# Performance work log

Hardware: AMD Instinct MI355X
Metric: run time of the kernel (lower is better)

The kernel has to match this reference:

```python
import jax, jax.numpy as jnp
import numpy as np

N_ENTITIES = 100000
EMBED = 64
BATCH = 4096
TEMPERATURE = 0.2


def _infonce(v1, v2, temperature):
    # v1, v2: [B, d]
    B = v1.shape[0]
    sim11 = v1 @ v1.T  # [B,B]
    sim22 = v2 @ v2.T
    sim12 = v1 @ v2.T
    eye = jnp.eye(B, dtype=bool)
    neg_inf = jnp.float32(-jnp.inf)
    sim11 = jnp.where(eye, neg_inf, sim11)
    sim22 = jnp.where(eye, neg_inf, sim22)
    logits1 = jnp.concatenate([sim12, sim11], axis=-1)          # [B,2B]
    logits2 = jnp.concatenate([sim22, sim12.T], axis=-1)        # [B,2B]
    logits = jnp.concatenate([logits1, logits2], axis=0) / temperature  # [2B,2B]
    targets = jnp.arange(2 * B)
    logp = jax.nn.log_softmax(logits, axis=-1)
    return -jnp.mean(jnp.take_along_axis(logp, targets[:, None], axis=-1))


def setup_inputs() -> dict:
    key = jax.random.key(0)
    k1, k2, k3, k4, k5, k6 = jax.random.split(key, 6)
    return {
        "input_u_list": jax.random.randint(k1, (BATCH,), 0, N_ENTITIES),
        "input_i_list": jax.random.randint(k2, (BATCH,), 0, N_ENTITIES),
        "u_sub1_embeddings": jax.random.normal(k3, (N_ENTITIES, EMBED), dtype=jnp.float32),
        "i_sub1_embeddings": jax.random.normal(k4, (N_ENTITIES, EMBED), dtype=jnp.float32),
        "u_sub2_embeddings": jax.random.normal(k5, (N_ENTITIES, EMBED), dtype=jnp.float32),
        "i_sub2_embeddings": jax.random.normal(k6, (N_ENTITIES, EMBED), dtype=jnp.float32),
    }


def reference(input_u_list, input_i_list, u_sub1_embeddings, i_sub1_embeddings,
              u_sub2_embeddings, i_sub2_embeddings):
    # user branch: gather + L2-normalize
    u1 = u_sub1_embeddings[input_u_list]
    u2 = u_sub2_embeddings[input_u_list]
    u1 = u1 / jnp.linalg.norm(u1, axis=1, keepdims=True)
    u2 = u2 / jnp.linalg.norm(u2, axis=1, keepdims=True)
    user_cl_loss = _infonce(u1, u2, TEMPERATURE)
    # item branch: gather only (the original does NOT normalize items)
    i1 = i_sub1_embeddings[input_i_list]
    i2 = i_sub2_embeddings[input_i_list]
    item_cl_loss = _infonce(i1, i2, TEMPERATURE)
    return user_cl_loss + item_cl_loss
```

## Files before the change

### kernel.cpp

```cpp
#include <hip/hip_runtime.h>
#include <hip/hip_bf16.h>
#include <math.h>

#define B_SZ   4096
#define D      64
#define RPB    8192
#define NCHUNK 8
#define TPC    8
#define NPART  16
#define LN2    0.69314718055994531f
#define PRESCALE 2.6857914f

typedef __attribute__((ext_vector_type(8))) short  bf16x8;
typedef __attribute__((ext_vector_type(4))) float  f32x4;

__device__ __forceinline__ float fexp2(float x) { return __builtin_amdgcn_exp2f(x); }


__global__ __launch_bounds__(256) void gather_kernel(
    const int* __restrict__ u_idx, const int* __restrict__ i_idx,
    const float* __restrict__ u1e, const float* __restrict__ i1e,
    const float* __restrict__ u2e, const float* __restrict__ i2e,
    __hip_bfloat16* __restrict__ Xbf, float* __restrict__ dots)
{
    const int tid  = threadIdx.x;
    const int wave = tid >> 6, lane = tid & 63;
    const int g      = blockIdx.x * 4 + wave;
    const int branch = g >> 12;
    const int i      = g & (B_SZ - 1);
    const int idx    = (branch == 0) ? u_idx[i] : i_idx[i];
    const float* s1  = (branch == 0) ? u1e : i1e;
    const float* s2  = (branch == 0) ? u2e : i2e;

    float v1 = s1[(size_t)idx * D + lane];
    float v2 = s2[(size_t)idx * D + lane];
    if (branch == 0) {
        float a = v1 * v1, b = v2 * v2;
        #pragma unroll
        for (int o = 32; o > 0; o >>= 1) {
            a += __shfl_xor(a, o, 64);
            b += __shfl_xor(b, o, 64);
        }
        v1 *= rsqrtf(a);
        v2 *= rsqrtf(b);
    }
    float p = v1 * v2;
    #pragma unroll
    for (int o = 32; o > 0; o >>= 1) p += __shfl_xor(p, o, 64);
    if (lane == 0) dots[g] = p;

    const size_t row1 = (size_t)branch * RPB + i;
    Xbf[row1 * D + lane]          = __float2bfloat16(v1 * PRESCALE);
    Xbf[(row1 + B_SZ) * D + lane] = __float2bfloat16(v2 * PRESCALE);
}

template<int IS_USER>
__device__ __forceinline__ void gram_body(
    const __hip_bfloat16* __restrict__ Xb, float2* __restrict__ P)
{
    const int tid   = threadIdx.x;
    const int bx    = blockIdx.x;
    const int chunk = blockIdx.y;
    const int r0    = bx * 128;

    const int wave = tid >> 6, lane = tid & 63;
    const int wm = wave >> 1, wn = wave & 1;
    const int quad = lane >> 4, tx = lane & 15;

    bf16x8 afr[4][2];
    const __hip_bfloat16* Ap = Xb + (size_t)(r0 + wm * 64 + tx) * D + quad * 8;
    #pragma unroll
    for (int mt = 0; mt < 4; ++mt)
        #pragma unroll
        for (int ks = 0; ks < 2; ++ks)
            afr[mt][ks] = *(const bf16x8*)(Ap + mt * 16 * D + ks * 32);

    float m_run[16], s_run[16];
    #pragma unroll
    for (int r = 0; r < 16; ++r) { m_run[r] = -INFINITY; s_run[r] = 0.f; }

    const int lrq  = wm * 64 + quad * 4;
    const int lcol = wn * 64 + tx;

    const __hip_bfloat16* Bbase =
        Xb + (size_t)(chunk * TPC * 128 + wn * 64 + tx) * D + quad * 8;

    for (int t = 0; t < TPC; ++t) {
        const int ct = chunk * TPC + t;
        const __hip_bfloat16* Bp = Bbase + (size_t)t * 128 * D;

        bf16x8 b0[4], b1[4];
        #pragma unroll
        for (int nt = 0; nt < 4; ++nt) {
            b0[nt] = *(const bf16x8*)(Bp + nt * 16 * D);
            b1[nt] = *(const bf16x8*)(Bp + nt * 16 * D + 32);
        }

        f32x4 acc[4][4];
        const f32x4 z = {0.f, 0.f, 0.f, 0.f};
        #pragma unroll
        for (int nt = 0; nt < 4; ++nt)
            #pragma unroll
            for (int mt = 0; mt < 4; ++mt)
                acc[mt][nt] = __builtin_amdgcn_mfma_f32_16x16x32_bf16(afr[mt][0], b0[nt], z, 0, 0, 0);
        #pragma unroll
        for (int nt = 0; nt < 4; ++nt)
            #pragma unroll
            for (int mt = 0; mt < 4; ++mt)
                acc[mt][nt] = __builtin_amdgcn_mfma_f32_16x16x32_bf16(afr[mt][1], b1[nt], acc[mt][nt], 0, 0, 0);

        const bool diag = (ct == bx);
        #pragma unroll
        for (int mt = 0; mt < 4; ++mt) {
            #pragma unroll
            for (int rr = 0; rr < 4; ++rr) {
                float y0 = acc[mt][0][rr], y1 = acc[mt][1][rr],
                      y2 = acc[mt][2][rr], y3 = acc[mt][3][rr];
                if (diag) {
                    const int dr = lrq + mt * 16 + rr - lcol;
                    if (dr == 0)  y0 = -INFINITY;
                    if (dr == 16) y1 = -INFINITY;
                    if (dr == 32) y2 = -INFINITY;
                    if (dr == 48) y3 = -INFINITY;
                }
                const int r = mt * 4 + rr;
                if (IS_USER) {
                    s_run[r] += fexp2(y0) + fexp2(y1) + fexp2(y2) + fexp2(y3);
                } else {
                    float mx   = fmaxf(fmaxf(y0, y1), fmaxf(y2, y3));
                    float newm = fmaxf(m_run[r], mx);
                    s_run[r] = s_run[r] * fexp2(m_run[r] - newm)
                             + fexp2(y0 - newm) + fexp2(y1 - newm)
                             + fexp2(y2 - newm) + fexp2(y3 - newm);
                    m_run[r] = newm;
                }
            }
        }
    }

    #pragma unroll
    for (int r = 0; r < 16; ++r) {
        float m = IS_USER ? 0.f : m_run[r];
        float s = s_run[r];
        #pragma unroll
        for (int o = 1; o < 16; o <<= 1) {
            if (IS_USER) {
                s += __shfl_xor(s, o, 64);
            } else {
                float om = __shfl_xor(m, o, 64);
                float os = __shfl_xor(s, o, 64);
                float M  = fmaxf(m, om);
                s = s * fexp2(m - M) + os * fexp2(om - M);
                m = M;
            }
        }
        if (tx == 0) {
            const int grow = r0 + wm * 64 + (r >> 2) * 16 + quad * 4 + (r & 3);
            P[(size_t)grow * NPART + chunk * 2 + wn] = make_float2(m, s);
        }
    }
}

__global__ __launch_bounds__(256, 3) void gram_lse_fused(
    const __hip_bfloat16* __restrict__ Xb0, float2* __restrict__ P0)
{
    const int branch = blockIdx.z;
    const __hip_bfloat16* Xb = Xb0 + (size_t)branch * RPB * D;
    float2* P = P0 + (size_t)branch * RPB * NPART;
    if (branch == 0) gram_body<1>(Xb, P);
    else             gram_body<0>(Xb, P);
}

__global__ __launch_bounds__(256) void merge_kernel(
    const float2* __restrict__ P, const float* __restrict__ dots,
    float* __restrict__ out)
{
    __shared__ float red[4];
    const int tid  = threadIdx.x;
    const int wave = tid >> 6, lane = tid & 63;

    float vsum = 0.f;
    #pragma unroll
    for (int k = 0; k < 8; ++k) {
        const int vb  = blockIdx.x * 8 + k;
        const int gw  = vb * 4 + wave;
        const int row = gw * 4 + (lane >> 4);
        const int c   = lane & 15;

        float2 p = P[(size_t)row * NPART + c];
        float m = p.x, s = p.y;
        #pragma unroll
        for (int o = 1; o < 16; o <<= 1) {
            float om = __shfl_xor(m, o, 64);
            float os = __shfl_xor(s, o, 64);
            float M  = fmaxf(m, om);
            s = s * fexp2(m - M) + os * fexp2(om - M);
            m = M;
        }

        if ((lane & 15) == 0)
            vsum += LN2 * (m + log2f(s)) * (1.0f / (float)RPB);
        if (tid < 8)
            vsum -= dots[vb * 8 + tid] * (5.0f / (float)B_SZ);
    }

    float v = vsum;
    #pragma unroll
    for (int o = 32; o > 0; o >>= 1) v += __shfl_xor(v, o, 64);
    if (lane == 0) red[wave] = v;
    __syncthreads();
    if (tid == 0)
        atomicAdd(out, red[0] + red[1] + red[2] + red[3]);
}

extern "C" void kernel_launch(void* const* d_in, const int* in_sizes, int n_in,
                              void* d_out, int out_size, void* d_ws, size_t ws_size,
                              hipStream_t stream) {
    const int*   u_idx = (const int*)d_in[0];
    const int*   i_idx = (const int*)d_in[1];
    const float* u1e   = (const float*)d_in[2];
    const float* i1e   = (const float*)d_in[3];
    const float* u2e   = (const float*)d_in[4];
    const float* i2e   = (const float*)d_in[5];
    float* out = (float*)d_out;

    __hip_bfloat16* Xbf = (__hip_bfloat16*)d_ws;
    float*  dots = (float*)((char*)d_ws + 2 * RPB * D * 2);
    float2* P    = (float2*)((char*)dots + RPB * sizeof(float));

    hipMemsetAsync(out, 0, sizeof(float), stream);

    gather_kernel<<<dim3(2048), dim3(256), 0, stream>>>(
        u_idx, i_idx, u1e, i1e, u2e, i2e, Xbf, dots);
    gram_lse_fused<<<dim3(64, NCHUNK, 2), dim3(256), 0, stream>>>(Xbf, P);
    merge_kernel<<<dim3(128), dim3(256), 0, stream>>>(P, dots, out);
}
```

Before: 173.3 us.

## Stage B tiles through double-buffered swizzled LDS with async global-to-LDS loads

In the gram kernel, each B column tile is now loaded once per block into LDS with global_load_lds, instead of every wave reading it straight from global memory. Two 16KB buffers let the next tile's load overlap the MFMA and exp work on the current one, and the row layout is XOR-swizzled to avoid bank conflicts. The grid is also rearranged so the user and item branches interleave along blockIdx.x. In exchange the kernel uses 32KB of shared memory per block, adds a barrier per tile, and forces the tile loop not to unroll, which may lower occupancy.

After: 169.2 us. 2.4% less time.

```diff
diff --git a/kernel.cpp b/kernel.cpp
--- a/kernel.cpp
+++ b/kernel.cpp
@@ -16,6 +16,12 @@
 
 __device__ __forceinline__ float fexp2(float x) { return __builtin_amdgcn_exp2f(x); }
 
+typedef const __attribute__((address_space(1))) unsigned int* gptr_t;
+typedef __attribute__((address_space(3))) unsigned int* lptr_t;
+__device__ __forceinline__ void stage16(const void* g, void* l) {
+    __builtin_amdgcn_global_load_lds((gptr_t)g, (lptr_t)l, 16, 0, 0);
+}
+
 
 __global__ __launch_bounds__(256) void gather_kernel(
     const int* __restrict__ u_idx, const int* __restrict__ i_idx,
@@ -56,10 +62,10 @@
 
 template<int IS_USER>
 __device__ __forceinline__ void gram_body(
-    const __hip_bfloat16* __restrict__ Xb, float2* __restrict__ P)
+    const __hip_bfloat16* __restrict__ Xb, float2* __restrict__ P,
+    const int bx, char* sm)
 {
     const int tid   = threadIdx.x;
-    const int bx    = blockIdx.x;
     const int chunk = blockIdx.y;
     const int r0    = bx * 128;
 
@@ -67,6 +73,18 @@
     const int wm = wave >> 1, wn = wave & 1;
     const int quad = lane >> 4, tx = lane & 15;
 
+    const int srow_b = wave * 32 + (lane >> 3);
+    const int scb    = ((lane & 7) * 16) ^ ((lane >> 3) << 4);
+    const char* Xbytes = (const char*)Xb;
+
+    {
+        const char* src = Xbytes + (size_t)(chunk * TPC) * 16384;
+        #pragma unroll
+        for (int k = 0; k < 4; ++k)
+            stage16(src + (srow_b + k * 8) * 128 + scb,
+                    sm + wave * 4096 + k * 1024);
+    }
+
     bf16x8 afr[4][2];
     const __hip_bfloat16* Ap = Xb + (size_t)(r0 + wm * 64 + tx) * D + quad * 8;
     #pragma unroll
@@ -82,18 +100,31 @@
     const int lrq  = wm * 64 + quad * 4;
     const int lcol = wn * 64 + tx;
 
-    const __hip_bfloat16* Bbase =
-        Xb + (size_t)(chunk * TPC * 128 + wn * 64 + tx) * D + quad * 8;
-
+    const int rbase = (wn * 64 + tx) * 128;
+    const int key   = (tx & 7) << 4;
+    const int cb0   = (quad * 16) ^ key;
+    const int cb1   = (64 + quad * 16) ^ key;
+
+    __syncthreads();
+
+    #pragma unroll 1
     for (int t = 0; t < TPC; ++t) {
-        const int ct = chunk * TPC + t;
-        const __hip_bfloat16* Bp = Bbase + (size_t)t * 128 * D;
+        const int ct  = chunk * TPC + t;
+        const int cur = (t & 1) << 14;
+
+        if (t + 1 < TPC) {
+            const char* src = Xbytes + (size_t)(ct + 1) * 16384;
+            char* dst = sm + (((t + 1) & 1) << 14) + wave * 4096;
+            #pragma unroll
+            for (int k = 0; k < 4; ++k)
+                stage16(src + (srow_b + k * 8) * 128 + scb, dst + k * 1024);
+        }
 
         bf16x8 b0[4], b1[4];
         #pragma unroll
         for (int nt = 0; nt < 4; ++nt) {
-            b0[nt] = *(const bf16x8*)(Bp + nt * 16 * D);
-            b1[nt] = *(const bf16x8*)(Bp + nt * 16 * D + 32);
+            b0[nt] = *(const bf16x8*)(sm + cur + rbase + nt * 2048 + cb0);
+            b1[nt] = *(const bf16x8*)(sm + cur + rbase + nt * 2048 + cb1);
         }
 
         f32x4 acc[4][4];
@@ -136,6 +167,8 @@
                 }
             }
         }
+
+        __syncthreads();
     }
 
     #pragma unroll
@@ -164,11 +197,13 @@
 __global__ __launch_bounds__(256, 3) void gram_lse_fused(
     const __hip_bfloat16* __restrict__ Xb0, float2* __restrict__ P0)
 {
-    const int branch = blockIdx.z;
+    __shared__ __align__(16) char sm[32768];
+    const int branch = blockIdx.x & 1;
+    const int bx     = blockIdx.x >> 1;
     const __hip_bfloat16* Xb = Xb0 + (size_t)branch * RPB * D;
     float2* P = P0 + (size_t)branch * RPB * NPART;
-    if (branch == 0) gram_body<1>(Xb, P);
-    else             gram_body<0>(Xb, P);
+    if (branch == 0) gram_body<1>(Xb, P, bx, sm);
+    else             gram_body<0>(Xb, P, bx, sm);
 }
 
 __global__ __launch_bounds__(256) void merge_kernel(
@@ -232,6 +267,6 @@
 
     gather_kernel<<<dim3(2048), dim3(256), 0, stream>>>(
         u_idx, i_idx, u1e, i1e, u2e, i2e, Xbf, dots);
-    gram_lse_fused<<<dim3(64, NCHUNK, 2), dim3(256), 0, stream>>>(Xbf, P);
+    gram_lse_fused<<<dim3(128, NCHUNK), dim3(256), 0, stream>>>(Xbf, P);
     merge_kernel<<<dim3(128), dim3(256), 0, stream>>>(P, dots, out);
 }
```
